# Kernel tuning notes

Measured on AMD Instinct MI355X. Metric: run time of the kernel, lower is better.

Reference implementation:

```python
import jax, jax.numpy as jnp
import numpy as np
import math

W_BITS = 256.0  # default w_bits in forward()

def ste_round(x):
    # straight-through estimator round: identity gradient
    return x + jax.lax.stop_gradient(jnp.round(x) - x)

def setup_inputs() -> dict:
    key = jax.random.key(0)
    k1, k2 = jax.random.split(key)
    x_size, y_size = 4096, 4096
    xb = jax.random.normal(k1, (8192, x_size), dtype=jnp.float32)
    W = jax.random.normal(k2, (x_size, y_size), dtype=jnp.float32) / math.sqrt(x_size)
    b = jnp.zeros((y_size,), dtype=jnp.float32)
    return {"xb": xb, "W": W, "b": b}

def reference(xb, W, b):
    # train=True path: fake-quant the weights (per-tensor symmetric int8), then matmul + bias
    s_w = 2.0 * jnp.max(jnp.abs(W)) / W_BITS          # per-tensor scale (zero-point 0)
    w_q = jnp.clip(ste_round(W / s_w), -127.0, 127.0)  # quantize + clamp
    w_fq = s_w * w_q                                    # dequantize (fake-quant)
    return xb @ w_fq + b
```

## Files before the change

kernel.cpp:

```cpp
#include <hip/hip_runtime.h>
#include <hip/hip_bf16.h>
#include <stdint.h>

typedef unsigned short u16;
typedef unsigned int u32;
typedef __bf16 bf16x8 __attribute__((ext_vector_type(8)));
typedef float f32x4 __attribute__((ext_vector_type(4)));
typedef u16 u16x4 __attribute__((ext_vector_type(4)));

typedef const __attribute__((address_space(1))) void* gas_ptr;
typedef __attribute__((address_space(3))) void* las_ptr;

#define M_DIM 8192
#define K_DIM 4096
#define N_DIM 4096

__device__ __forceinline__ u16 f32_to_bf16_rne(float f) {
    u32 u = __float_as_uint(f);
    u += 0x7FFFu + ((u >> 16) & 1u);
    return (u16)(u >> 16);
}

__global__ void maxabs_kernel(const float* __restrict__ W, u32* __restrict__ out, int n4) {
    int idx = blockIdx.x * blockDim.x + threadIdx.x;
    int stride = gridDim.x * blockDim.x;
    const float4* W4 = (const float4*)W;
    float m = 0.0f;
    for (int i = idx; i < n4; i += stride) {
        float4 v = W4[i];
        m = fmaxf(m, fmaxf(fmaxf(fabsf(v.x), fabsf(v.y)), fmaxf(fabsf(v.z), fabsf(v.w))));
    }
#pragma unroll
    for (int off = 32; off > 0; off >>= 1)
        m = fmaxf(m, __shfl_down(m, off));
    if ((threadIdx.x & 63) == 0)
        atomicMax(out, __float_as_uint(m));
}

__global__ void quant_transpose_kernel(const float* __restrict__ W, u16* __restrict__ Wt,
                                       const u32* __restrict__ mb) {
    __shared__ u16 tile[32][33];
    const float s_inv = 128.0f / __uint_as_float(*mb);
    int n = blockIdx.x * 32 + threadIdx.x;
#pragma unroll
    for (int r = threadIdx.y; r < 32; r += 8) {
        int k = blockIdx.y * 32 + r;
        float q = rintf(W[(size_t)k * N_DIM + n] * s_inv);
        q = fminf(fmaxf(q, -127.0f), 127.0f);
        tile[threadIdx.x][r] = (u16)(__float_as_uint(q) >> 16);
    }
    __syncthreads();
    int k_out = blockIdx.y * 32 + threadIdx.x;
#pragma unroll
    for (int r = threadIdx.y; r < 32; r += 8) {
        int n_out = blockIdx.x * 32 + r;
        Wt[(size_t)n_out * K_DIM + k_out] = tile[r][threadIdx.x];
    }
}

__global__ void cast_bf16_kernel(const float* __restrict__ x, u16* __restrict__ y, int n4) {
    int idx = blockIdx.x * blockDim.x + threadIdx.x;
    int stride = gridDim.x * blockDim.x;
    const float4* x4 = (const float4*)x;
    u16x4* y4 = (u16x4*)y;
    for (int i = idx; i < n4; i += stride) {
        float4 v = x4[i];
        u16x4 o;
        o.x = f32_to_bf16_rne(v.x);
        o.y = f32_to_bf16_rne(v.y);
        o.z = f32_to_bf16_rne(v.z);
        o.w = f32_to_bf16_rne(v.w);
        y4[i] = o;
    }
}

__global__ __launch_bounds__(256) void gemm_kernel(const u16* __restrict__ A,
                                                   const u16* __restrict__ Bt,
                                                   const float* __restrict__ bias,
                                                   const u32* __restrict__ mb,
                                                   float* __restrict__ out) {
    __shared__ u16 As[128 * 32];
    __shared__ u16 Bs[128 * 32];

    const int tid = threadIdx.x;
    const int wave = tid >> 6;
    const int lane = tid & 63;
    const int m0 = blockIdx.y * 128;
    const int n0 = blockIdx.x * 128;

    const int lrow = lane >> 2;
    const int lcol = (lane & 3) * 8;

    const u16* Ag0 = A + (size_t)(m0 + wave * 16 + lrow) * K_DIM + lcol;
    const u16* Ag1 = A + (size_t)(m0 + (wave + 4) * 16 + lrow) * K_DIM + lcol;
    const u16* Bg0 = Bt + (size_t)(n0 + wave * 16 + lrow) * K_DIM + lcol;
    const u16* Bg1 = Bt + (size_t)(n0 + (wave + 4) * 16 + lrow) * K_DIM + lcol;

    u16* Asl0 = &As[wave * 512];
    u16* Asl1 = &As[(wave + 4) * 512];
    u16* Bsl0 = &Bs[wave * 512];
    u16* Bsl1 = &Bs[(wave + 4) * 512];

    const int quad = lane >> 4;
    const int l15 = lane & 15;
    const int wm = wave >> 1;
    const int wn = wave & 1;

    const float s_w = __uint_as_float(*mb) * (1.0f / 128.0f);

    f32x4 acc[4][4];
#pragma unroll
    for (int i = 0; i < 4; i++)
#pragma unroll
        for (int j = 0; j < 4; j++) acc[i][j] = (f32x4){0.f, 0.f, 0.f, 0.f};

    for (int k0 = 0; k0 < K_DIM; k0 += 32) {
        __syncthreads();
        __builtin_amdgcn_global_load_lds((gas_ptr)(Ag0 + k0), (las_ptr)Asl0, 16, 0, 0);
        __builtin_amdgcn_global_load_lds((gas_ptr)(Ag1 + k0), (las_ptr)Asl1, 16, 0, 0);
        __builtin_amdgcn_global_load_lds((gas_ptr)(Bg0 + k0), (las_ptr)Bsl0, 16, 0, 0);
        __builtin_amdgcn_global_load_lds((gas_ptr)(Bg1 + k0), (las_ptr)Bsl1, 16, 0, 0);
        __syncthreads();

        bf16x8 af[4], bfr[4];
#pragma unroll
        for (int i = 0; i < 4; i++)
            af[i] = *(const bf16x8*)&As[(wm * 64 + i * 16 + l15) * 32 + quad * 8];
#pragma unroll
        for (int j = 0; j < 4; j++)
            bfr[j] = *(const bf16x8*)&Bs[(wn * 64 + j * 16 + l15) * 32 + quad * 8];

#pragma unroll
        for (int i = 0; i < 4; i++)
#pragma unroll
            for (int j = 0; j < 4; j++)
                acc[i][j] = __builtin_amdgcn_mfma_f32_16x16x32_bf16(af[i], bfr[j], acc[i][j], 0, 0, 0);
    }

#pragma unroll
    for (int j = 0; j < 4; j++) {
        const int col = n0 + wn * 64 + j * 16 + l15;
        const float bv = bias[col];
#pragma unroll
        for (int i = 0; i < 4; i++) {
            const int row = m0 + wm * 64 + i * 16 + quad * 4;
            float* op = out + (size_t)row * N_DIM + col;
#pragma unroll
            for (int r = 0; r < 4; r++) op[(size_t)r * N_DIM] = s_w * acc[i][j][r] + bv;
        }
    }
}

extern "C" void kernel_launch(void* const* d_in, const int* in_sizes, int n_in,
                              void* d_out, int out_size, void* d_ws, size_t ws_size,
                              hipStream_t stream) {
    const float* xb = (const float*)d_in[0];
    const float* W = (const float*)d_in[1];
    const float* b = (const float*)d_in[2];
    float* out = (float*)d_out;

    u32* mb = (u32*)d_ws;
    u16* xb_bf = (u16*)((char*)d_ws + 256);
    u16* wqt = (u16*)((char*)d_ws + 256 + (size_t)M_DIM * K_DIM * 2);

    hipMemsetAsync(d_ws, 0, 4, stream);
    maxabs_kernel<<<1024, 256, 0, stream>>>(W, mb, (K_DIM * N_DIM) / 4);
    quant_transpose_kernel<<<dim3(N_DIM / 32, K_DIM / 32), dim3(32, 8), 0, stream>>>(W, wqt, mb);
    cast_bf16_kernel<<<4096, 256, 0, stream>>>(xb, xb_bf, (M_DIM * K_DIM) / 4);
    gemm_kernel<<<dim3(N_DIM / 128, M_DIM / 128), 256, 0, stream>>>(xb_bf, wqt, b, mb, out);
}
```

Baseline: 637.0 us.

## Use 32x32 MFMA with BK=64 swizzled LDS and fuse prep kernels

```diff
diff --git a/kernel.cpp b/kernel.cpp
--- a/kernel.cpp
+++ b/kernel.cpp
@@ -5,7 +5,7 @@
 typedef unsigned short u16;
 typedef unsigned int u32;
 typedef __bf16 bf16x8 __attribute__((ext_vector_type(8)));
-typedef float f32x4 __attribute__((ext_vector_type(4)));
+typedef float f32x16 __attribute__((ext_vector_type(16)));
 typedef u16 u16x4 __attribute__((ext_vector_type(4)));
 
 typedef const __attribute__((address_space(1))) void* gas_ptr;
@@ -14,6 +14,7 @@
 #define M_DIM 8192
 #define K_DIM 4096
 #define N_DIM 4096
+#define BK 64
 
 __device__ __forceinline__ u16 f32_to_bf16_rne(float f) {
     u32 u = __float_as_uint(f);
@@ -21,12 +22,14 @@
     return (u16)(u >> 16);
 }
 
-__global__ void maxabs_kernel(const float* __restrict__ W, u32* __restrict__ out, int n4) {
+__global__ void prep_kernel(const float* __restrict__ W, u32* __restrict__ mb,
+                            const float* __restrict__ x, u16* __restrict__ y) {
     int idx = blockIdx.x * blockDim.x + threadIdx.x;
     int stride = gridDim.x * blockDim.x;
+
     const float4* W4 = (const float4*)W;
     float m = 0.0f;
-    for (int i = idx; i < n4; i += stride) {
+    for (int i = idx; i < (K_DIM * N_DIM) / 4; i += stride) {
         float4 v = W4[i];
         m = fmaxf(m, fmaxf(fmaxf(fabsf(v.x), fabsf(v.y)), fmaxf(fabsf(v.z), fabsf(v.w))));
     }
@@ -34,36 +37,11 @@
     for (int off = 32; off > 0; off >>= 1)
         m = fmaxf(m, __shfl_down(m, off));
     if ((threadIdx.x & 63) == 0)
-        atomicMax(out, __float_as_uint(m));
-}
+        atomicMax(mb, __float_as_uint(m));
 
-__global__ void quant_transpose_kernel(const float* __restrict__ W, u16* __restrict__ Wt,
-                                       const u32* __restrict__ mb) {
-    __shared__ u16 tile[32][33];
-    const float s_inv = 128.0f / __uint_as_float(*mb);
-    int n = blockIdx.x * 32 + threadIdx.x;
-#pragma unroll
-    for (int r = threadIdx.y; r < 32; r += 8) {
-        int k = blockIdx.y * 32 + r;
-        float q = rintf(W[(size_t)k * N_DIM + n] * s_inv);
-        q = fminf(fmaxf(q, -127.0f), 127.0f);
-        tile[threadIdx.x][r] = (u16)(__float_as_uint(q) >> 16);
-    }
-    __syncthreads();
-    int k_out = blockIdx.y * 32 + threadIdx.x;
-#pragma unroll
-    for (int r = threadIdx.y; r < 32; r += 8) {
-        int n_out = blockIdx.x * 32 + r;
-        Wt[(size_t)n_out * K_DIM + k_out] = tile[r][threadIdx.x];
-    }
-}
-
-__global__ void cast_bf16_kernel(const float* __restrict__ x, u16* __restrict__ y, int n4) {
-    int idx = blockIdx.x * blockDim.x + threadIdx.x;
-    int stride = gridDim.x * blockDim.x;
     const float4* x4 = (const float4*)x;
     u16x4* y4 = (u16x4*)y;
-    for (int i = idx; i < n4; i += stride) {
+    for (int i = idx; i < (M_DIM * K_DIM) / 4; i += stride) {
         float4 v = x4[i];
         u16x4 o;
         o.x = f32_to_bf16_rne(v.x);
@@ -74,13 +52,46 @@
     }
 }
 
+__global__ __launch_bounds__(256) void quant_transpose_kernel(const float* __restrict__ W,
+                                                              u16* __restrict__ Wt,
+                                                              const u32* __restrict__ mb) {
+    __shared__ u16 tileT[64][68];
+    const float s_inv = 128.0f / __uint_as_float(*mb);
+    const int t = threadIdx.x;
+    const int k0 = blockIdx.y * 64, n0 = blockIdx.x * 64;
+    const int c4 = t & 15;
+    const int r = t >> 4;
+#pragma unroll
+    for (int p = 0; p < 4; p++) {
+        int kl = p * 16 + r;
+        float4 v = *(const float4*)&W[(size_t)(k0 + kl) * N_DIM + n0 + c4 * 4];
+        float q0 = fminf(fmaxf(rintf(v.x * s_inv), -127.f), 127.f);
+        float q1 = fminf(fmaxf(rintf(v.y * s_inv), -127.f), 127.f);
+        float q2 = fminf(fmaxf(rintf(v.z * s_inv), -127.f), 127.f);
+        float q3 = fminf(fmaxf(rintf(v.w * s_inv), -127.f), 127.f);
+        tileT[c4 * 4 + 0][kl] = (u16)(__float_as_uint(q0) >> 16);
+        tileT[c4 * 4 + 1][kl] = (u16)(__float_as_uint(q1) >> 16);
+        tileT[c4 * 4 + 2][kl] = (u16)(__float_as_uint(q2) >> 16);
+        tileT[c4 * 4 + 3][kl] = (u16)(__float_as_uint(q3) >> 16);
+    }
+    __syncthreads();
+    const int k4 = t & 15;
+    const int nr = t >> 4;
+#pragma unroll
+    for (int p = 0; p < 4; p++) {
+        int nl = p * 16 + nr;
+        u16x4 v = *(const u16x4*)&tileT[nl][k4 * 4];
+        *(u16x4*)&Wt[(size_t)(n0 + nl) * K_DIM + k0 + k4 * 4] = v;
+    }
+}
+
 __global__ __launch_bounds__(256) void gemm_kernel(const u16* __restrict__ A,
                                                    const u16* __restrict__ Bt,
                                                    const float* __restrict__ bias,
                                                    const u32* __restrict__ mb,
                                                    float* __restrict__ out) {
-    __shared__ u16 As[128 * 32];
-    __shared__ u16 Bs[128 * 32];
+    __shared__ u16 As[128 * BK];
+    __shared__ u16 Bs[128 * BK];
 
     const int tid = threadIdx.x;
     const int wave = tid >> 6;
@@ -88,65 +99,77 @@
     const int m0 = blockIdx.y * 128;
     const int n0 = blockIdx.x * 128;
 
-    const int lrow = lane >> 2;
-    const int lcol = (lane & 3) * 8;
+    const int srow = lane >> 3;
+    const int schunk = (lane & 7) ^ srow;
 
-    const u16* Ag0 = A + (size_t)(m0 + wave * 16 + lrow) * K_DIM + lcol;
-    const u16* Ag1 = A + (size_t)(m0 + (wave + 4) * 16 + lrow) * K_DIM + lcol;
-    const u16* Bg0 = Bt + (size_t)(n0 + wave * 16 + lrow) * K_DIM + lcol;
-    const u16* Bg1 = Bt + (size_t)(n0 + (wave + 4) * 16 + lrow) * K_DIM + lcol;
+    const u16* Ag[4];
+    const u16* Bg[4];
+    u16* Asl[4];
+    u16* Bsl[4];
+#pragma unroll
+    for (int c = 0; c < 4; c++) {
+        int g = wave * 4 + c;
+        Ag[c] = A + (size_t)(m0 + g * 8 + srow) * K_DIM + schunk * 8;
+        Bg[c] = Bt + (size_t)(n0 + g * 8 + srow) * K_DIM + schunk * 8;
+        Asl[c] = &As[g * 512];
+        Bsl[c] = &Bs[g * 512];
+    }
 
-    u16* Asl0 = &As[wave * 512];
-    u16* Asl1 = &As[(wave + 4) * 512];
-    u16* Bsl0 = &Bs[wave * 512];
-    u16* Bsl1 = &Bs[(wave + 4) * 512];
-
-    const int quad = lane >> 4;
-    const int l15 = lane & 15;
     const int wm = wave >> 1;
     const int wn = wave & 1;
+    const int l31 = lane & 31;
+    const int lhi = lane >> 5;
 
     const float s_w = __uint_as_float(*mb) * (1.0f / 128.0f);
 
-    f32x4 acc[4][4];
+    f32x16 acc[2][2];
 #pragma unroll
-    for (int i = 0; i < 4; i++)
+    for (int i = 0; i < 2; i++)
 #pragma unroll
-        for (int j = 0; j < 4; j++) acc[i][j] = (f32x4){0.f, 0.f, 0.f, 0.f};
+        for (int j = 0; j < 2; j++)
+#pragma unroll
+            for (int r = 0; r < 16; r++) acc[i][j][r] = 0.0f;
 
-    for (int k0 = 0; k0 < K_DIM; k0 += 32) {
+    const int ar0 = (wm * 64 + l31) * BK;
+    const int ar1 = (wm * 64 + 32 + l31) * BK;
+    const int br0 = (wn * 64 + l31) * BK;
+    const int br1 = (wn * 64 + 32 + l31) * BK;
+
+    for (int k0 = 0; k0 < K_DIM; k0 += BK) {
         __syncthreads();
-        __builtin_amdgcn_global_load_lds((gas_ptr)(Ag0 + k0), (las_ptr)Asl0, 16, 0, 0);
-        __builtin_amdgcn_global_load_lds((gas_ptr)(Ag1 + k0), (las_ptr)Asl1, 16, 0, 0);
-        __builtin_amdgcn_global_load_lds((gas_ptr)(Bg0 + k0), (las_ptr)Bsl0, 16, 0, 0);
-        __builtin_amdgcn_global_load_lds((gas_ptr)(Bg1 + k0), (las_ptr)Bsl1, 16, 0, 0);
+#pragma unroll
+        for (int c = 0; c < 4; c++) {
+            __builtin_amdgcn_global_load_lds((gas_ptr)(Ag[c] + k0), (las_ptr)Asl[c], 16, 0, 0);
+            __builtin_amdgcn_global_load_lds((gas_ptr)(Bg[c] + k0), (las_ptr)Bsl[c], 16, 0, 0);
+        }
         __syncthreads();
 
-        bf16x8 af[4], bfr[4];
 #pragma unroll
-        for (int i = 0; i < 4; i++)
-            af[i] = *(const bf16x8*)&As[(wm * 64 + i * 16 + l15) * 32 + quad * 8];
-#pragma unroll
-        for (int j = 0; j < 4; j++)
-            bfr[j] = *(const bf16x8*)&Bs[(wn * 64 + j * 16 + l15) * 32 + quad * 8];
-
-#pragma unroll
-        for (int i = 0; i < 4; i++)
-#pragma unroll
-            for (int j = 0; j < 4; j++)
-                acc[i][j] = __builtin_amdgcn_mfma_f32_16x16x32_bf16(af[i], bfr[j], acc[i][j], 0, 0, 0);
+        for (int s = 0; s < 4; s++) {
+            const int p = ((s << 1) + lhi) ^ (lane & 7);
+            bf16x8 a0 = *(const bf16x8*)&As[ar0 + p * 8];
+            bf16x8 a1 = *(const bf16x8*)&As[ar1 + p * 8];
+            bf16x8 b0 = *(const bf16x8*)&Bs[br0 + p * 8];
+            bf16x8 b1 = *(const bf16x8*)&Bs[br1 + p * 8];
+            acc[0][0] = __builtin_amdgcn_mfma_f32_32x32x16_bf16(a0, b0, acc[0][0], 0, 0, 0);
+            acc[0][1] = __builtin_amdgcn_mfma_f32_32x32x16_bf16(a0, b1, acc[0][1], 0, 0, 0);
+            acc[1][0] = __builtin_amdgcn_mfma_f32_32x32x16_bf16(a1, b0, acc[1][0], 0, 0, 0);
+            acc[1][1] = __builtin_amdgcn_mfma_f32_32x32x16_bf16(a1, b1, acc[1][1], 0, 0, 0);
+        }
     }
 
 #pragma unroll
-    for (int j = 0; j < 4; j++) {
-        const int col = n0 + wn * 64 + j * 16 + l15;
+    for (int j = 0; j < 2; j++) {
+        const int col = n0 + wn * 64 + j * 32 + l31;
         const float bv = bias[col];
 #pragma unroll
-        for (int i = 0; i < 4; i++) {
-            const int row = m0 + wm * 64 + i * 16 + quad * 4;
-            float* op = out + (size_t)row * N_DIM + col;
+        for (int i = 0; i < 2; i++) {
+            const int rbase = m0 + wm * 64 + i * 32 + 4 * lhi;
 #pragma unroll
-            for (int r = 0; r < 4; r++) op[(size_t)r * N_DIM] = s_w * acc[i][j][r] + bv;
+            for (int r = 0; r < 16; r++) {
+                const int row = rbase + (r & 3) + 8 * (r >> 2);
+                out[(size_t)row * N_DIM + col] = s_w * acc[i][j][r] + bv;
+            }
         }
     }
 }
@@ -164,8 +187,7 @@
     u16* wqt = (u16*)((char*)d_ws + 256 + (size_t)M_DIM * K_DIM * 2);
 
     hipMemsetAsync(d_ws, 0, 4, stream);
-    maxabs_kernel<<<1024, 256, 0, stream>>>(W, mb, (K_DIM * N_DIM) / 4);
-    quant_transpose_kernel<<<dim3(N_DIM / 32, K_DIM / 32), dim3(32, 8), 0, stream>>>(W, wqt, mb);
-    cast_bf16_kernel<<<4096, 256, 0, stream>>>(xb, xb_bf, (M_DIM * K_DIM) / 4);
+    prep_kernel<<<2048, 256, 0, stream>>>(W, mb, xb, xb_bf);
+    quant_transpose_kernel<<<dim3(N_DIM / 64, K_DIM / 64), 256, 0, stream>>>(W, wqt, mb);
     gemm_kernel<<<dim3(N_DIM / 128, M_DIM / 128), 256, 0, stream>>>(xb_bf, wqt, b, mb, out);
 }
```

Measured after the change: 665.9 us. +4.5%, slower.
